# Optimization experiments

Measured on AMD Instinct MI355X. Metric: run time of the kernel, lower is better.

Reference implementation:

```python
import jax, jax.numpy as jnp
import numpy as np

EPS = 1e-6  # torch GaussianNLLLoss default eps


def _linear_params(key, in_size, out_size):
    # torch nn.Linear default init: U(-1/sqrt(in), 1/sqrt(in)) for W and b
    kw, kb = jax.random.split(key)
    bound = 1.0 / np.sqrt(in_size)
    W = jax.random.uniform(kw, (out_size, in_size), minval=-bound, maxval=bound, dtype=jnp.float32)
    b = jax.random.uniform(kb, (out_size,), minval=-bound, maxval=bound, dtype=jnp.float32)
    return W, b


def setup_inputs() -> dict:
    key = jax.random.key(0)
    B, IN, H = 32768, 512, 512
    ks = jax.random.split(key, 6)
    x = jax.random.normal(ks[0], (B, IN), dtype=jnp.float32)
    y = jax.random.normal(ks[1], (B, IN), dtype=jnp.float32)
    W_mu_x, b_mu_x = _linear_params(ks[2], IN, H)
    W_sg_x, b_sg_x = _linear_params(ks[3], IN, H)
    W_mu_y, b_mu_y = _linear_params(ks[4], IN, H)
    W_sg_y, b_sg_y = _linear_params(ks[5], IN, H)
    return {"x": x, "y": y,
            "W_mu_x": W_mu_x, "b_mu_x": b_mu_x,
            "W_sg_x": W_sg_x, "b_sg_x": b_sg_x,
            "W_mu_y": W_mu_y, "b_mu_y": b_mu_y,
            "W_sg_y": W_sg_y, "b_sg_y": b_sg_y}


def _gaussian_nll(xi, mean, var):
    # torch GaussianNLLLoss (full=False, reduction='mean'):
    # mean over features of 0.5*(log(max(var,eps)) + (xi-mean)^2/max(var,eps))
    v = jnp.maximum(var, EPS)
    return 0.5 * jnp.mean(jnp.log(v) + (xi - mean) ** 2 / v)


def _sample_row(key, mx, my, vx, vy):
    # rejection sampling: draw u~U(0,1), xi~U(-1,1); accept when u >= q(xi)
    def cond(c):
        return jnp.logical_not(c[2])

    def body(c):
        k = c[0]
        k, k1, k2 = jax.random.split(k, 3)
        u = jax.random.uniform(k1, dtype=jnp.float32)
        xi = 2.0 * jax.random.uniform(k2, dtype=jnp.float32) - 1.0
        q = _gaussian_nll(xi, mx, vx) * _gaussian_nll(xi, my, vy)
        return (k, xi, u >= q)

    _, xi, _ = jax.lax.while_loop(cond, body, (key, jnp.float32(0.0), jnp.bool_(False)))
    return xi


def reference(x, y, W_mu_x, b_mu_x, W_sg_x, b_sg_x, W_mu_y, b_mu_y, W_sg_y, b_sg_y):
    mean_x = x @ W_mu_x.T + b_mu_x          # [B, H]
    mean_y = y @ W_mu_y.T + b_mu_y          # [B, H]
    std_x = jnp.exp(x @ W_sg_x.T + b_sg_x)  # [B, H] (used as 'var' in GaussianNLLLoss)
    std_y = jnp.exp(y @ W_sg_y.T + b_sg_y)  # [B, H]
    B = x.shape[0]
    keys = jax.random.split(jax.random.key(42), B)
    X = jax.vmap(_sample_row)(keys, mean_x, mean_y, std_x, std_y)  # [B]
    return jnp.clip(X, 1e-5, 10.0)
```

## Files before the change

kernel.cpp:

```cpp
#include <hip/hip_runtime.h>
#include <stdint.h>
#include <math.h>


typedef _Float16 f16;
typedef __attribute__((ext_vector_type(8))) _Float16 f16x8;
typedef __attribute__((ext_vector_type(4))) _Float16 f16x4;
typedef __attribute__((ext_vector_type(4))) float f32x4;

#define SX 16.0f
#define SW 1024.0f
#define INV_S (1.0f / 16384.0f)
#define LOG_EPS (-13.815510557964274f)
#define PLANE 262144
#define WS_NEED (4u * 2u * PLANE * 2u)

struct U2 { uint32_t a, b; };

__device__ __forceinline__ uint32_t rotl(uint32_t v, int d) {
  return (v << d) | (v >> (32 - d));
}

__device__ __forceinline__ U2 tf2x32(uint32_t k0, uint32_t k1, uint32_t x0, uint32_t x1) {
  const uint32_t k2 = k0 ^ k1 ^ 0x1BD11BDAu;
  x0 += k0; x1 += k1;
#define TFR(r) { x0 += x1; x1 = rotl(x1, r); x1 ^= x0; }
  TFR(13) TFR(15) TFR(26) TFR(6)
  x0 += k1; x1 += k2 + 1u;
  TFR(17) TFR(29) TFR(16) TFR(24)
  x0 += k2; x1 += k0 + 2u;
  TFR(13) TFR(15) TFR(26) TFR(6)
  x0 += k0; x1 += k1 + 3u;
  TFR(17) TFR(29) TFR(16) TFR(24)
  x0 += k1; x1 += k2 + 4u;
  TFR(13) TFR(15) TFR(26) TFR(6)
  x0 += k2; x1 += k0 + 5u;
#undef TFR
  U2 r; r.a = x0; r.b = x1; return r;
}

__device__ __forceinline__ float bits_to_u01(uint32_t b) {
  return __uint_as_float((b >> 9) | 0x3f800000u) - 1.0f;
}

__global__ __launch_bounds__(256) void convert_w_kernel(
    const float* __restrict__ w0, const float* __restrict__ w1,
    const float* __restrict__ w2, const float* __restrict__ w3,
    f16* __restrict__ ws)
{
  const int mat = blockIdx.x >> 8;
  const int idx = (((blockIdx.x & 255) << 8) | threadIdx.x) << 2;
  const float* W = (mat == 0) ? w0 : (mat == 1) ? w1 : (mat == 2) ? w2 : w3;
  float4 v = *(const float4*)(W + idx);
  f16* hi = ws + (size_t)mat * (2 * PLANE) + idx;
  f16* lo = hi + PLANE;
  float a0 = v.x * SW, a1 = v.y * SW, a2 = v.z * SW, a3 = v.w * SW;
  f16 h0 = (f16)a0, h1 = (f16)a1, h2 = (f16)a2, h3 = (f16)a3;
  *(f16x4*)hi = (f16x4){h0, h1, h2, h3};
  *(f16x4*)lo = (f16x4){(f16)(a0 - (float)h0), (f16)(a1 - (float)h1),
                        (f16)(a2 - (float)h2), (f16)(a3 - (float)h3)};
}

__device__ __forceinline__ int swz_off(int row, int quad) {
  return row * 32 + ((quad ^ ((row >> 1) & 3)) << 3);
}

__global__ __launch_bounds__(256, 2)
void mfma_proposal_kernel(const float* __restrict__ gx, const float* __restrict__ gy,
                          const float* __restrict__ bmux, const float* __restrict__ bsgx,
                          const float* __restrict__ bmuy, const float* __restrict__ bsgy,
                          const f16* __restrict__ ws, float* __restrict__ out)
{
  __shared__ f16 Xh[64 * 32], Xl[64 * 32];
  __shared__ f16 Wp[4][128 * 32];
  __shared__ double red[4][64][8];

  const int tid = threadIdx.x;
  const int lane = tid & 63;
  const int w = tid >> 6;
  const int ln = lane & 15;
  const int quad = lane >> 4;
  const int r0 = blockIdx.x * 64;

  const int xrow = tid >> 2;
  const int xs4 = tid & 3;
  const int dma_sg = (lane & 3) ^ ((lane >> 3) & 3);
  const int dma_row = lane >> 2;

  for (int i = tid; i < 4 * 64 * 8; i += 256) (&red[0][0][0])[i] = 0.0;

  const float* xbase = gx + (size_t)(r0 + xrow) * 512 + xs4 * 8;
  float4 xr0 = *(const float4*)(xbase);
  float4 xr1 = *(const float4*)(xbase + 4);

  f32x4 accm[4][2], accv[4][2];

  for (int rid = 0; rid < 128; ++rid) {
    const int kc = rid & 15;
    const int cg = (rid >> 4) & 3;
    const int dist = rid >> 6;

    if (kc == 0) {
#pragma unroll
      for (int ri = 0; ri < 4; ++ri)
#pragma unroll
        for (int cj = 0; cj < 2; ++cj) {
          accm[ri][cj] = (f32x4)0.0f;
          accv[ri][cj] = (f32x4)0.0f;
        }
    }

    __syncthreads();

    {
      const f16* plane = ws + (size_t)(dist * 2 + (w >> 1)) * (2 * PLANE)
                            + (size_t)(w & 1) * PLANE;
      const int k0 = kc * 32;
      const int c0 = cg * 128;
      const f16* gp0 = plane + (size_t)(c0 + dma_row) * 512 + k0 + dma_sg * 8;
#pragma unroll
      for (int j = 0; j < 8; ++j) {
        const f16* gp = gp0 + (size_t)(j * 16) * 512;
        f16* lp = &Wp[w][(j * 16) * 32];
        __builtin_amdgcn_global_load_lds(
            (const __attribute__((address_space(1))) void*)gp,
            (__attribute__((address_space(3))) void*)lp, 16, 0, 0);
      }
    }

    {
      const int slot = ((xs4 ^ ((xrow >> 1) & 3)) << 3);
      float a0 = xr0.x * SX, a1 = xr0.y * SX, a2 = xr0.z * SX, a3 = xr0.w * SX;
      float a4 = xr1.x * SX, a5 = xr1.y * SX, a6 = xr1.z * SX, a7 = xr1.w * SX;
      f16 h0 = (f16)a0, h1 = (f16)a1, h2 = (f16)a2, h3 = (f16)a3;
      f16 h4 = (f16)a4, h5 = (f16)a5, h6 = (f16)a6, h7 = (f16)a7;
      *(f16x8*)&Xh[xrow * 32 + slot] = (f16x8){h0, h1, h2, h3, h4, h5, h6, h7};
      *(f16x8*)&Xl[xrow * 32 + slot] =
          (f16x8){(f16)(a0 - (float)h0), (f16)(a1 - (float)h1),
                  (f16)(a2 - (float)h2), (f16)(a3 - (float)h3),
                  (f16)(a4 - (float)h4), (f16)(a5 - (float)h5),
                  (f16)(a6 - (float)h6), (f16)(a7 - (float)h7)};
    }

    __syncthreads();

    if (rid + 1 < 128) {
      const int n = rid + 1;
      const float* Xg = (n >> 6) ? gy : gx;
      const float* xp = Xg + (size_t)(r0 + xrow) * 512 + (n & 15) * 32 + xs4 * 8;
      xr0 = *(const float4*)(xp);
      xr1 = *(const float4*)(xp + 4);
    }

    f16x8 ah[4], al[4];
#pragma unroll
    for (int ri = 0; ri < 4; ++ri) {
      const int off = swz_off(ri * 16 + ln, quad);
      ah[ri] = *(const f16x8*)&Xh[off];
      al[ri] = *(const f16x8*)&Xl[off];
    }
#pragma unroll
    for (int cj = 0; cj < 2; ++cj) {
      const int boff = swz_off(w * 32 + cj * 16 + ln, quad);
      const f16x8 bhm = *(const f16x8*)&Wp[0][boff];
      const f16x8 blm = *(const f16x8*)&Wp[1][boff];
      const f16x8 bhv = *(const f16x8*)&Wp[2][boff];
      const f16x8 blv = *(const f16x8*)&Wp[3][boff];
#pragma unroll
      for (int ri = 0; ri < 4; ++ri) {
        accm[ri][cj] = __builtin_amdgcn_mfma_f32_16x16x32_f16(al[ri], bhm, accm[ri][cj], 0, 0, 0);
        accm[ri][cj] = __builtin_amdgcn_mfma_f32_16x16x32_f16(ah[ri], blm, accm[ri][cj], 0, 0, 0);
        accm[ri][cj] = __builtin_amdgcn_mfma_f32_16x16x32_f16(ah[ri], bhm, accm[ri][cj], 0, 0, 0);
        accv[ri][cj] = __builtin_amdgcn_mfma_f32_16x16x32_f16(al[ri], bhv, accv[ri][cj], 0, 0, 0);
        accv[ri][cj] = __builtin_amdgcn_mfma_f32_16x16x32_f16(ah[ri], blv, accv[ri][cj], 0, 0, 0);
        accv[ri][cj] = __builtin_amdgcn_mfma_f32_16x16x32_f16(ah[ri], bhv, accv[ri][cj], 0, 0, 0);
      }
    }

    if (kc == 15) {
      const float* bmu = dist ? bmuy : bmux;
      const float* bsg = dist ? bsgy : bsgx;
      float bm0 = bmu[cg * 128 + w * 32 + ln];
      float bm1 = bmu[cg * 128 + w * 32 + 16 + ln];
      float bv0 = bsg[cg * 128 + w * 32 + ln];
      float bv1 = bsg[cg * 128 + w * 32 + 16 + ln];
#pragma unroll
      for (int ri = 0; ri < 4; ++ri) {
#pragma unroll
        for (int g = 0; g < 4; ++g) {
          float pA = 0.f, pI = 0.f, pM = 0.f, pQ = 0.f;
#pragma unroll
          for (int cj = 0; cj < 2; ++cj) {
            const float m = accm[ri][cj][g] * INV_S + (cj ? bm1 : bm0);
            const float s = accv[ri][cj][g] * INV_S + (cj ? bv1 : bv0);
            const float vv = fmaxf(expf(s), 1e-6f);
            const float lg = fmaxf(s, LOG_EPS);
            const float iv = __builtin_amdgcn_rcpf(vv);
            pA += lg;
            pI += iv;
            pM += m * iv;
            pQ += m * m * iv;
          }
#pragma unroll
          for (int msk = 1; msk < 16; msk <<= 1) {
            pA += __shfl_xor(pA, msk);
            pI += __shfl_xor(pI, msk);
            pM += __shfl_xor(pM, msk);
            pQ += __shfl_xor(pQ, msk);
          }
          if (ln == 0) {
            double* rr = &red[w][ri * 16 + quad * 4 + g][dist * 4];
            rr[0] += (double)pA; rr[1] += (double)pI;
            rr[2] += (double)pM; rr[3] += (double)pQ;
          }
        }
      }
    }
  }

  __syncthreads();

  if (tid < 64) {
    const int grow = r0 + tid;
    double Ax = 0, Ix = 0, Mx = 0, Qx = 0, Ay = 0, Iy = 0, My = 0, Qy = 0;
#pragma unroll
    for (int s = 0; s < 4; ++s) {
      Ax += red[s][tid][0]; Ix += red[s][tid][1];
      Mx += red[s][tid][2]; Qx += red[s][tid][3];
      Ay += red[s][tid][4]; Iy += red[s][tid][5];
      My += red[s][tid][6]; Qy += red[s][tid][7];
    }

    U2 key = tf2x32(0u, 42u, 0u, (uint32_t)grow);

    float xi = 0.0f;
    bool done = false;
    for (int it = 0; it < 100000 && !done; ++it) {
      const U2 kn = tf2x32(key.a, key.b, 0u, 0u);
      const U2 k1 = tf2x32(key.a, key.b, 0u, 1u);
      const U2 k2 = tf2x32(key.a, key.b, 0u, 2u);
      const U2 ru = tf2x32(k1.a, k1.b, 0u, 0u);
      const U2 rx = tf2x32(k2.a, k2.b, 0u, 0u);
      const float u  = bits_to_u01(ru.a ^ ru.b);
      const float u2 = bits_to_u01(rx.a ^ rx.b);
      xi = 2.0f * u2 - 1.0f;
      const double dxi = (double)xi;
      const double nx = (0.5 / 512.0) * (Ax + Qx + dxi * (dxi * Ix - 2.0 * Mx));
      const double ny = (0.5 / 512.0) * (Ay + Qy + dxi * (dxi * Iy - 2.0 * My));
      done = ((double)u >= nx * ny);
      key = kn;
    }
    out[grow] = fminf(fmaxf(xi, 1e-5f), 10.0f);
  }
}

__global__ __launch_bounds__(256, 1)
void fused_proposal_vec(const float* __restrict__ gx, const float* __restrict__ gy,
                        const float* __restrict__ Wmux, const float* __restrict__ bmux,
                        const float* __restrict__ Wsgx, const float* __restrict__ bsgx,
                        const float* __restrict__ Wmuy, const float* __restrict__ bmuy,
                        const float* __restrict__ Wsgy, const float* __restrict__ bsgy,
                        float* __restrict__ out)
{
  __shared__ float Xs[16][68];
  __shared__ float Wms[16][132];
  __shared__ float Wss[16][132];
  __shared__ double red[64][8];

  const int tid = threadIdx.x;
  const int tx = tid & 15;
  const int ty = tid >> 4;
  const int r0 = blockIdx.x * 64;
  const int lr = tid >> 2;
  const int q4 = (tid & 3) << 2;

  for (int i = tid; i < 64 * 8; i += 256) ((double*)red)[i] = 0.0;

  for (int ph = 0; ph < 8; ++ph) {
    const int dist = ph >> 2;
    const int c0 = (ph & 3) * 128;
    const float* __restrict__ Xg = dist ? gy : gx;
    const float* __restrict__ Wm = dist ? Wmuy : Wmux;
    const float* __restrict__ Wv = dist ? Wsgy : Wsgx;
    const float* __restrict__ bm = dist ? bmuy : bmux;
    const float* __restrict__ bv = dist ? bsgy : bsgx;

    float am[4][8], av[4][8];
#pragma unroll
    for (int r = 0; r < 4; ++r)
#pragma unroll
      for (int c = 0; c < 8; ++c) { am[r][c] = 0.0f; av[r][c] = 0.0f; }

    const float* xp  = Xg + (size_t)(r0 + lr) * 512 + q4;
    const float* mp0 = Wm + (size_t)(c0 + lr) * 512 + q4;
    const float* mp1 = Wm + (size_t)(c0 + lr + 64) * 512 + q4;
    const float* vp0 = Wv + (size_t)(c0 + lr) * 512 + q4;
    const float* vp1 = Wv + (size_t)(c0 + lr + 64) * 512 + q4;

    float4 xa = *(const float4*)(xp);
    float4 ma = *(const float4*)(mp0);
    float4 mb = *(const float4*)(mp1);
    float4 va = *(const float4*)(vp0);
    float4 vb = *(const float4*)(vp1);

    for (int t = 0; t < 32; ++t) {
      __syncthreads();
#define ST4(arr, col, v) { arr[q4+0][col]=v.x; arr[q4+1][col]=v.y; arr[q4+2][col]=v.z; arr[q4+3][col]=v.w; }
      ST4(Xs,  lr, xa)
      ST4(Wms, lr, ma)  ST4(Wms, lr + 64, mb)
      ST4(Wss, lr, va)  ST4(Wss, lr + 64, vb)
#undef ST4
      __syncthreads();
      if (t + 1 < 32) {
        const int ko = (t + 1) * 16;
        xa = *(const float4*)(xp + ko);
        ma = *(const float4*)(mp0 + ko);
        mb = *(const float4*)(mp1 + ko);
        va = *(const float4*)(vp0 + ko);
        vb = *(const float4*)(vp1 + ko);
      }
#pragma unroll
      for (int kk = 0; kk < 16; ++kk) {
        const float4 x0 = *(const float4*)&Xs[kk][ty * 4];
        const float4 m0 = *(const float4*)&Wms[kk][tx * 4];
        const float4 m1 = *(const float4*)&Wms[kk][tx * 4 + 64];
        const float4 v0 = *(const float4*)&Wss[kk][tx * 4];
        const float4 v1 = *(const float4*)&Wss[kk][tx * 4 + 64];
        const float xr[4] = {x0.x, x0.y, x0.z, x0.w};
        const float wm[8] = {m0.x, m0.y, m0.z, m0.w, m1.x, m1.y, m1.z, m1.w};
        const float wv[8] = {v0.x, v0.y, v0.z, v0.w, v1.x, v1.y, v1.z, v1.w};
#pragma unroll
        for (int r = 0; r < 4; ++r)
#pragma unroll
          for (int c = 0; c < 8; ++c) {
            am[r][c] = fmaf(xr[r], wm[c], am[r][c]);
            av[r][c] = fmaf(xr[r], wv[c], av[r][c]);
          }
      }
    }

    float bmr[8], bvr[8];
#pragma unroll
    for (int c = 0; c < 4; ++c) {
      bmr[c]     = bm[c0 + tx * 4 + c];
      bmr[4 + c] = bm[c0 + 64 + tx * 4 + c];
      bvr[c]     = bv[c0 + tx * 4 + c];
      bvr[4 + c] = bv[c0 + 64 + tx * 4 + c];
    }
#pragma unroll
    for (int r = 0; r < 4; ++r) {
      float pA = 0.f, pI = 0.f, pM = 0.f, pQ = 0.f;
#pragma unroll
      for (int c = 0; c < 8; ++c) {
        const float m = am[r][c] + bmr[c];
        const float s = av[r][c] + bvr[c];
        const float v = fmaxf(expf(s), 1e-6f);
        const float lg = fmaxf(s, LOG_EPS);
        const float inv = __builtin_amdgcn_rcpf(v);
        pA += lg; pI += inv; pM += m * inv; pQ += m * m * inv;
      }
#pragma unroll
      for (int msk = 1; msk < 16; msk <<= 1) {
        pA += __shfl_xor(pA, msk);
        pI += __shfl_xor(pI, msk);
        pM += __shfl_xor(pM, msk);
        pQ += __shfl_xor(pQ, msk);
      }
      if (tx == 0) {
        double* rr = &red[ty * 4 + r][dist * 4];
        rr[0] += (double)pA; rr[1] += (double)pI;
        rr[2] += (double)pM; rr[3] += (double)pQ;
      }
    }
  }

  __syncthreads();

  if (tid < 64) {
    const int grow = r0 + tid;
    const double Ax = red[tid][0], Ix = red[tid][1], Mx = red[tid][2], Qx = red[tid][3];
    const double Ay = red[tid][4], Iy = red[tid][5], My = red[tid][6], Qy = red[tid][7];
    U2 key = tf2x32(0u, 42u, 0u, (uint32_t)grow);
    float xi = 0.0f;
    bool done = false;
    for (int it = 0; it < 100000 && !done; ++it) {
      const U2 kn = tf2x32(key.a, key.b, 0u, 0u);
      const U2 k1 = tf2x32(key.a, key.b, 0u, 1u);
      const U2 k2 = tf2x32(key.a, key.b, 0u, 2u);
      const U2 ru = tf2x32(k1.a, k1.b, 0u, 0u);
      const U2 rx = tf2x32(k2.a, k2.b, 0u, 0u);
      const float u  = bits_to_u01(ru.a ^ ru.b);
      const float u2 = bits_to_u01(rx.a ^ rx.b);
      xi = 2.0f * u2 - 1.0f;
      const double dxi = (double)xi;
      const double nx = (0.5 / 512.0) * (Ax + Qx + dxi * (dxi * Ix - 2.0 * Mx));
      const double ny = (0.5 / 512.0) * (Ay + Qy + dxi * (dxi * Iy - 2.0 * My));
      done = ((double)u >= nx * ny);
      key = kn;
    }
    out[grow] = fminf(fmaxf(xi, 1e-5f), 10.0f);
  }
}

extern "C" void kernel_launch(void* const* d_in, const int* in_sizes, int n_in,
                              void* d_out, int out_size, void* d_ws, size_t ws_size,
                              hipStream_t stream) {
  const float* x    = (const float*)d_in[0];
  const float* y    = (const float*)d_in[1];
  const float* Wmux = (const float*)d_in[2];
  const float* bmux = (const float*)d_in[3];
  const float* Wsgx = (const float*)d_in[4];
  const float* bsgx = (const float*)d_in[5];
  const float* Wmuy = (const float*)d_in[6];
  const float* bmuy = (const float*)d_in[7];
  const float* Wsgy = (const float*)d_in[8];
  const float* bsgy = (const float*)d_in[9];
  (void)in_sizes; (void)n_in; (void)out_size;

  if (ws_size >= (size_t)WS_NEED) {
    convert_w_kernel<<<1024, 256, 0, stream>>>(Wmux, Wsgx, Wmuy, Wsgy, (f16*)d_ws);
    mfma_proposal_kernel<<<512, 256, 0, stream>>>(
        x, y, bmux, bsgx, bmuy, bsgy, (const f16*)d_ws, (float*)d_out);
  } else {
    fused_proposal_vec<<<512, 256, 0, stream>>>(
        x, y, Wmux, bmux, Wsgx, bsgx, Wmuy, bmuy, Wsgy, bsgy, (float*)d_out);
  }
}
```

Measured before the change: 394.4 us.

## Double-buffer weight and input tiles in LDS, keep row reductions in registers

Adds ping-pong LDS buffers for the weight and split-f16 input tiles, so the next k-chunk is staged while the current one is consumed by MFMA. This replaces the two barriers per iteration with a single wait plus barrier. The per-row statistics are now kept in double registers on a designated lane instead of being added into a shared reduction array, and that array is aliased onto the weight buffer at the end. LDS use per block roughly doubles, which may limit the two-blocks-per-CU occupancy target, and the explicit vmcnt(0) wait still serialises on the prefetch.

```diff
diff --git a/kernel.cpp b/kernel.cpp
--- a/kernel.cpp
+++ b/kernel.cpp
@@ -71,9 +71,9 @@
                           const float* __restrict__ bmuy, const float* __restrict__ bsgy,
                           const f16* __restrict__ ws, float* __restrict__ out)
 {
-  __shared__ f16 Xh[64 * 32], Xl[64 * 32];
-  __shared__ f16 Wp[4][128 * 32];
-  __shared__ double red[4][64][8];
+  __shared__ __align__(16) f16 Wp[2][4][128 * 32];
+  __shared__ __align__(16) f16 Xh[2][64 * 32];
+  __shared__ __align__(16) f16 Xl[2][64 * 32];
 
   const int tid = threadIdx.x;
   const int lane = tid & 63;
@@ -86,16 +86,57 @@
   const int xs4 = tid & 3;
   const int dma_sg = (lane & 3) ^ ((lane >> 3) & 3);
   const int dma_row = lane >> 2;
-
-  for (int i = tid; i < 4 * 64 * 8; i += 256) (&red[0][0][0])[i] = 0.0;
-
-  const float* xbase = gx + (size_t)(r0 + xrow) * 512 + xs4 * 8;
-  float4 xr0 = *(const float4*)(xbase);
-  float4 xr1 = *(const float4*)(xbase + 4);
+  const int xslot = (xs4 ^ ((xrow >> 1) & 3)) << 3;
+
+  double dAx = 0, dIx = 0, dMx = 0, dQx = 0;
+  double dAy = 0, dIy = 0, dMy = 0, dQy = 0;
+
+  float4 xr0, xr1;
+
+  auto load_xr = [&](int n) {
+    const float* Xg = (n >> 6) ? gy : gx;
+    const float* xp = Xg + (size_t)(r0 + xrow) * 512 + (n & 15) * 32 + xs4 * 8;
+    xr0 = *(const float4*)(xp);
+    xr1 = *(const float4*)(xp + 4);
+  };
+
+  auto stage_w = [&](int n, int buf) {
+    const int nkc = n & 15, ncg = (n >> 4) & 3, nd = n >> 6;
+    const f16* plane = ws + (size_t)(nd * 2 + (w >> 1)) * (2 * PLANE)
+                          + (size_t)(w & 1) * PLANE;
+    const f16* gp0 = plane + (size_t)(ncg * 128 + dma_row) * 512 + nkc * 32 + dma_sg * 8;
+#pragma unroll
+    for (int j = 0; j < 8; ++j) {
+      __builtin_amdgcn_global_load_lds(
+          (const __attribute__((address_space(1))) void*)(gp0 + (size_t)(j * 16) * 512),
+          (__attribute__((address_space(3))) void*)&Wp[buf][w][(j * 16) * 32], 16, 0, 0);
+    }
+  };
+
+  auto write_x = [&](int buf) {
+    float a0 = xr0.x * SX, a1 = xr0.y * SX, a2 = xr0.z * SX, a3 = xr0.w * SX;
+    float a4 = xr1.x * SX, a5 = xr1.y * SX, a6 = xr1.z * SX, a7 = xr1.w * SX;
+    f16 h0 = (f16)a0, h1 = (f16)a1, h2 = (f16)a2, h3 = (f16)a3;
+    f16 h4 = (f16)a4, h5 = (f16)a5, h6 = (f16)a6, h7 = (f16)a7;
+    *(f16x8*)&Xh[buf][xrow * 32 + xslot] = (f16x8){h0, h1, h2, h3, h4, h5, h6, h7};
+    *(f16x8*)&Xl[buf][xrow * 32 + xslot] =
+        (f16x8){(f16)(a0 - (float)h0), (f16)(a1 - (float)h1),
+                (f16)(a2 - (float)h2), (f16)(a3 - (float)h3),
+                (f16)(a4 - (float)h4), (f16)(a5 - (float)h5),
+                (f16)(a6 - (float)h6), (f16)(a7 - (float)h7)};
+  };
+
+  load_xr(0);
+  stage_w(0, 0);
+  write_x(0);
+  load_xr(1);
+  __syncthreads();
 
   f32x4 accm[4][2], accv[4][2];
 
   for (int rid = 0; rid < 128; ++rid) {
+    const int cb = rid & 1;
+    const int nb = cb ^ 1;
     const int kc = rid & 15;
     const int cg = (rid >> 4) & 3;
     const int dist = rid >> 6;
@@ -110,62 +151,26 @@
         }
     }
 
-    __syncthreads();
-
-    {
-      const f16* plane = ws + (size_t)(dist * 2 + (w >> 1)) * (2 * PLANE)
-                            + (size_t)(w & 1) * PLANE;
-      const int k0 = kc * 32;
-      const int c0 = cg * 128;
-      const f16* gp0 = plane + (size_t)(c0 + dma_row) * 512 + k0 + dma_sg * 8;
-#pragma unroll
-      for (int j = 0; j < 8; ++j) {
-        const f16* gp = gp0 + (size_t)(j * 16) * 512;
-        f16* lp = &Wp[w][(j * 16) * 32];
-        __builtin_amdgcn_global_load_lds(
-            (const __attribute__((address_space(1))) void*)gp,
-            (__attribute__((address_space(3))) void*)lp, 16, 0, 0);
-      }
-    }
-
-    {
-      const int slot = ((xs4 ^ ((xrow >> 1) & 3)) << 3);
-      float a0 = xr0.x * SX, a1 = xr0.y * SX, a2 = xr0.z * SX, a3 = xr0.w * SX;
-      float a4 = xr1.x * SX, a5 = xr1.y * SX, a6 = xr1.z * SX, a7 = xr1.w * SX;
-      f16 h0 = (f16)a0, h1 = (f16)a1, h2 = (f16)a2, h3 = (f16)a3;
-      f16 h4 = (f16)a4, h5 = (f16)a5, h6 = (f16)a6, h7 = (f16)a7;
-      *(f16x8*)&Xh[xrow * 32 + slot] = (f16x8){h0, h1, h2, h3, h4, h5, h6, h7};
-      *(f16x8*)&Xl[xrow * 32 + slot] =
-          (f16x8){(f16)(a0 - (float)h0), (f16)(a1 - (float)h1),
-                  (f16)(a2 - (float)h2), (f16)(a3 - (float)h3),
-                  (f16)(a4 - (float)h4), (f16)(a5 - (float)h5),
-                  (f16)(a6 - (float)h6), (f16)(a7 - (float)h7)};
-    }
-
-    __syncthreads();
-
     if (rid + 1 < 128) {
-      const int n = rid + 1;
-      const float* Xg = (n >> 6) ? gy : gx;
-      const float* xp = Xg + (size_t)(r0 + xrow) * 512 + (n & 15) * 32 + xs4 * 8;
-      xr0 = *(const float4*)(xp);
-      xr1 = *(const float4*)(xp + 4);
-    }
+      stage_w(rid + 1, nb);
+      write_x(nb);
+    }
+    if (rid + 2 < 128) load_xr(rid + 2);
 
     f16x8 ah[4], al[4];
 #pragma unroll
     for (int ri = 0; ri < 4; ++ri) {
       const int off = swz_off(ri * 16 + ln, quad);
-      ah[ri] = *(const f16x8*)&Xh[off];
-      al[ri] = *(const f16x8*)&Xl[off];
+      ah[ri] = *(const f16x8*)&Xh[cb][off];
+      al[ri] = *(const f16x8*)&Xl[cb][off];
     }
 #pragma unroll
     for (int cj = 0; cj < 2; ++cj) {
       const int boff = swz_off(w * 32 + cj * 16 + ln, quad);
-      const f16x8 bhm = *(const f16x8*)&Wp[0][boff];
-      const f16x8 blm = *(const f16x8*)&Wp[1][boff];
-      const f16x8 bhv = *(const f16x8*)&Wp[2][boff];
-      const f16x8 blv = *(const f16x8*)&Wp[3][boff];
+      const f16x8 bhm = *(const f16x8*)&Wp[cb][0][boff];
+      const f16x8 blm = *(const f16x8*)&Wp[cb][1][boff];
+      const f16x8 bhv = *(const f16x8*)&Wp[cb][2][boff];
+      const f16x8 blv = *(const f16x8*)&Wp[cb][3][boff];
 #pragma unroll
       for (int ri = 0; ri < 4; ++ri) {
         accm[ri][cj] = __builtin_amdgcn_mfma_f32_16x16x32_f16(al[ri], bhm, accm[ri][cj], 0, 0, 0);
@@ -180,10 +185,10 @@
     if (kc == 15) {
       const float* bmu = dist ? bmuy : bmux;
       const float* bsg = dist ? bsgy : bsgx;
-      float bm0 = bmu[cg * 128 + w * 32 + ln];
-      float bm1 = bmu[cg * 128 + w * 32 + 16 + ln];
-      float bv0 = bsg[cg * 128 + w * 32 + ln];
-      float bv1 = bsg[cg * 128 + w * 32 + 16 + ln];
+      const float bm0 = bmu[cg * 128 + w * 32 + ln];
+      const float bm1 = bmu[cg * 128 + w * 32 + 16 + ln];
+      const float bv0 = bsg[cg * 128 + w * 32 + ln];
+      const float bv1 = bsg[cg * 128 + w * 32 + 16 + ln];
 #pragma unroll
       for (int ri = 0; ri < 4; ++ri) {
 #pragma unroll
@@ -208,16 +213,27 @@
             pM += __shfl_xor(pM, msk);
             pQ += __shfl_xor(pQ, msk);
           }
-          if (ln == 0) {
-            double* rr = &red[w][ri * 16 + quad * 4 + g][dist * 4];
-            rr[0] += (double)pA; rr[1] += (double)pI;
-            rr[2] += (double)pM; rr[3] += (double)pQ;
+          if (ln == ri * 4 + g) {
+            if (dist == 0) { dAx += pA; dIx += pI; dMx += pM; dQx += pQ; }
+            else           { dAy += pA; dIy += pI; dMy += pM; dQy += pQ; }
           }
         }
       }
     }
-  }
-
+
+    asm volatile("s_waitcnt vmcnt(0)" ::: "memory");
+    asm volatile("s_waitcnt lgkmcnt(0)" ::: "memory");
+    __builtin_amdgcn_s_barrier();
+  }
+
+  __syncthreads();
+  double* red = (double*)&Wp[0][0][0];
+  {
+    const int myrow = (ln >> 2) * 16 + quad * 4 + (ln & 3);
+    double* rr = red + (size_t)(w * 64 + myrow) * 8;
+    rr[0] = dAx; rr[1] = dIx; rr[2] = dMx; rr[3] = dQx;
+    rr[4] = dAy; rr[5] = dIy; rr[6] = dMy; rr[7] = dQy;
+  }
   __syncthreads();
 
   if (tid < 64) {
@@ -225,10 +241,9 @@
     double Ax = 0, Ix = 0, Mx = 0, Qx = 0, Ay = 0, Iy = 0, My = 0, Qy = 0;
 #pragma unroll
     for (int s = 0; s < 4; ++s) {
-      Ax += red[s][tid][0]; Ix += red[s][tid][1];
-      Mx += red[s][tid][2]; Qx += red[s][tid][3];
-      Ay += red[s][tid][4]; Iy += red[s][tid][5];
-      My += red[s][tid][6]; Qy += red[s][tid][7];
+      const double* rr = red + (size_t)(s * 64 + tid) * 8;
+      Ax += rr[0]; Ix += rr[1]; Mx += rr[2]; Qx += rr[3];
+      Ay += rr[4]; Iy += rr[5]; My += rr[6]; Qy += rr[7];
     }
 
     U2 key = tf2x32(0u, 42u, 0u, (uint32_t)grow);
```

New measurement: 430.3 us. +9.1%, slower.

## Pre-swizzle weights into MFMA fragment layout and load B operands directly to registers

Applied to the files above, without the earlier changes.

The weight conversion kernel now writes the f16 hi/lo split in the exact per-lane MFMA B-fragment order. The main kernel therefore drops the LDS weight staging buffer and the global_load_lds DMA, loading B fragments straight into registers. These loads are double-buffered, so the next round's fragments are fetched while the current round's MFMAs run. This removes LDS traffic and shared memory for weights, which may raise occupancy. The cost is more VGPRs for the two fragment buffers and every wave reading its fragments from global/L2 memory.

```diff
diff --git a/kernel.cpp b/kernel.cpp
--- a/kernel.cpp
+++ b/kernel.cpp
@@ -5,7 +5,6 @@
 
 typedef _Float16 f16;
 typedef __attribute__((ext_vector_type(8))) _Float16 f16x8;
-typedef __attribute__((ext_vector_type(4))) _Float16 f16x4;
 typedef __attribute__((ext_vector_type(4))) float f32x4;
 
 #define SX 16.0f
@@ -14,6 +13,13 @@
 #define LOG_EPS (-13.815510557964274f)
 #define PLANE 262144
 #define WS_NEED (4u * 2u * PLANE * 2u)
+
+#define KC_S   512
+#define CJ_S   8192
+#define WV_S   16384
+#define CG_S   65536
+#define HILO_S 262144
+#define MAT_S  524288
 
 struct U2 { uint32_t a, b; };
 
@@ -48,17 +54,34 @@
     const float* __restrict__ w2, const float* __restrict__ w3,
     f16* __restrict__ ws)
 {
-  const int mat = blockIdx.x >> 8;
-  const int idx = (((blockIdx.x & 255) << 8) | threadIdx.x) << 2;
+  const int t = blockIdx.x * 256 + threadIdx.x;
+  const int mat = t >> 15;
+  const int r = t & 32767;
+  const int lane = r & 63;
+  const int kc = (r >> 6) & 15;
+  const int cj = (r >> 10) & 1;
+  const int wv = (r >> 11) & 3;
+  const int cg = (r >> 13) & 3;
+  const int ln = lane & 15, quad = lane >> 4;
+  const int row = cg * 128 + wv * 32 + cj * 16 + ln;
+  const int k0 = kc * 32 + quad * 8;
   const float* W = (mat == 0) ? w0 : (mat == 1) ? w1 : (mat == 2) ? w2 : w3;
-  float4 v = *(const float4*)(W + idx);
-  f16* hi = ws + (size_t)mat * (2 * PLANE) + idx;
-  f16* lo = hi + PLANE;
-  float a0 = v.x * SW, a1 = v.y * SW, a2 = v.z * SW, a3 = v.w * SW;
-  f16 h0 = (f16)a0, h1 = (f16)a1, h2 = (f16)a2, h3 = (f16)a3;
-  *(f16x4*)hi = (f16x4){h0, h1, h2, h3};
-  *(f16x4*)lo = (f16x4){(f16)(a0 - (float)h0), (f16)(a1 - (float)h1),
-                        (f16)(a2 - (float)h2), (f16)(a3 - (float)h3)};
+  const float* p = W + (size_t)row * 512 + k0;
+  const float4 va = *(const float4*)p;
+  const float4 vb = *(const float4*)(p + 4);
+  const float a[8] = {va.x, va.y, va.z, va.w, vb.x, vb.y, vb.z, vb.w};
+  f16x8 h, l;
+#pragma unroll
+  for (int i = 0; i < 8; ++i) {
+    const float ai = a[i] * SW;
+    const f16 hi = (f16)ai;
+    h[i] = hi;
+    l[i] = (f16)(ai - (float)hi);
+  }
+  f16* dst = ws + (size_t)mat * MAT_S + (size_t)cg * CG_S + (size_t)wv * WV_S
+                + (size_t)cj * CJ_S + (size_t)kc * KC_S + (size_t)lane * 8;
+  *(f16x8*)dst = h;
+  *(f16x8*)(dst + HILO_S) = l;
 }
 
 __device__ __forceinline__ int swz_off(int row, int quad) {
@@ -72,7 +95,6 @@
                           const f16* __restrict__ ws, float* __restrict__ out)
 {
   __shared__ f16 Xh[64 * 32], Xl[64 * 32];
-  __shared__ f16 Wp[4][128 * 32];
   __shared__ double red[4][64][8];
 
   const int tid = threadIdx.x;
@@ -84,18 +106,53 @@
 
   const int xrow = tid >> 2;
   const int xs4 = tid & 3;
-  const int dma_sg = (lane & 3) ^ ((lane >> 3) & 3);
-  const int dma_row = lane >> 2;
+  const int xslot = (xs4 ^ ((xrow >> 1) & 3)) << 3;
 
   for (int i = tid; i < 4 * 64 * 8; i += 256) (&red[0][0][0])[i] = 0.0;
 
-  const float* xbase = gx + (size_t)(r0 + xrow) * 512 + xs4 * 8;
-  float4 xr0 = *(const float4*)(xbase);
-  float4 xr1 = *(const float4*)(xbase + 4);
-
+  const f16* wbase = ws + (size_t)w * WV_S + (size_t)lane * 8;
+
+  float4 xr0, xr1;
+  auto load_xr = [&](int n) {
+    const float* Xg = (n >> 6) ? gy : gx;
+    const float* xp = Xg + (size_t)(r0 + xrow) * 512 + (n & 15) * 32 + xs4 * 8;
+    xr0 = *(const float4*)(xp);
+    xr1 = *(const float4*)(xp + 4);
+  };
+
+  auto write_x = [&]() {
+    float a0 = xr0.x * SX, a1 = xr0.y * SX, a2 = xr0.z * SX, a3 = xr0.w * SX;
+    float a4 = xr1.x * SX, a5 = xr1.y * SX, a6 = xr1.z * SX, a7 = xr1.w * SX;
+    f16 h0 = (f16)a0, h1 = (f16)a1, h2 = (f16)a2, h3 = (f16)a3;
+    f16 h4 = (f16)a4, h5 = (f16)a5, h6 = (f16)a6, h7 = (f16)a7;
+    *(f16x8*)&Xh[xrow * 32 + xslot] = (f16x8){h0, h1, h2, h3, h4, h5, h6, h7};
+    *(f16x8*)&Xl[xrow * 32 + xslot] =
+        (f16x8){(f16)(a0 - (float)h0), (f16)(a1 - (float)h1),
+                (f16)(a2 - (float)h2), (f16)(a3 - (float)h3),
+                (f16)(a4 - (float)h4), (f16)(a5 - (float)h5),
+                (f16)(a6 - (float)h6), (f16)(a7 - (float)h7)};
+  };
+
+  auto load_W = [&](int n, f16x8 (&B)[4][2]) {
+    const int kc = n & 15, cg = (n >> 4) & 3, d = n >> 6;
+    const f16* base = wbase + (size_t)(d * 2) * MAT_S + (size_t)cg * CG_S
+                            + (size_t)kc * KC_S;
+#pragma unroll
+    for (int p = 0; p < 4; ++p)
+#pragma unroll
+      for (int cj = 0; cj < 2; ++cj)
+        B[p][cj] = *(const f16x8*)(base + (size_t)(p >> 1) * MAT_S
+                                        + (size_t)(p & 1) * HILO_S
+                                        + (size_t)cj * CJ_S);
+  };
+
+  f16x8 Ba[4][2], Bb[4][2];
   f32x4 accm[4][2], accv[4][2];
 
-  for (int rid = 0; rid < 128; ++rid) {
+  load_xr(0);
+  load_W(0, Ba);
+
+  auto round_fn = [&](int rid, f16x8 (&Bc)[4][2], f16x8 (&Bn)[4][2]) {
     const int kc = rid & 15;
     const int cg = (rid >> 4) & 3;
     const int dist = rid >> 6;
@@ -111,45 +168,12 @@
     }
 
     __syncthreads();
-
-    {
-      const f16* plane = ws + (size_t)(dist * 2 + (w >> 1)) * (2 * PLANE)
-                            + (size_t)(w & 1) * PLANE;
-      const int k0 = kc * 32;
-      const int c0 = cg * 128;
-      const f16* gp0 = plane + (size_t)(c0 + dma_row) * 512 + k0 + dma_sg * 8;
-#pragma unroll
-      for (int j = 0; j < 8; ++j) {
-        const f16* gp = gp0 + (size_t)(j * 16) * 512;
-        f16* lp = &Wp[w][(j * 16) * 32];
-        __builtin_amdgcn_global_load_lds(
-            (const __attribute__((address_space(1))) void*)gp,
-            (__attribute__((address_space(3))) void*)lp, 16, 0, 0);
-      }
-    }
-
-    {
-      const int slot = ((xs4 ^ ((xrow >> 1) & 3)) << 3);
-      float a0 = xr0.x * SX, a1 = xr0.y * SX, a2 = xr0.z * SX, a3 = xr0.w * SX;
-      float a4 = xr1.x * SX, a5 = xr1.y * SX, a6 = xr1.z * SX, a7 = xr1.w * SX;
-      f16 h0 = (f16)a0, h1 = (f16)a1, h2 = (f16)a2, h3 = (f16)a3;
-      f16 h4 = (f16)a4, h5 = (f16)a5, h6 = (f16)a6, h7 = (f16)a7;
-      *(f16x8*)&Xh[xrow * 32 + slot] = (f16x8){h0, h1, h2, h3, h4, h5, h6, h7};
-      *(f16x8*)&Xl[xrow * 32 + slot] =
-          (f16x8){(f16)(a0 - (float)h0), (f16)(a1 - (float)h1),
-                  (f16)(a2 - (float)h2), (f16)(a3 - (float)h3),
-                  (f16)(a4 - (float)h4), (f16)(a5 - (float)h5),
-                  (f16)(a6 - (float)h6), (f16)(a7 - (float)h7)};
-    }
-
+    write_x();
     __syncthreads();
 
     if (rid + 1 < 128) {
-      const int n = rid + 1;
-      const float* Xg = (n >> 6) ? gy : gx;
-      const float* xp = Xg + (size_t)(r0 + xrow) * 512 + (n & 15) * 32 + xs4 * 8;
-      xr0 = *(const float4*)(xp);
-      xr1 = *(const float4*)(xp + 4);
+      load_xr(rid + 1);
+      load_W(rid + 1, Bn);
     }
 
     f16x8 ah[4], al[4];
@@ -161,11 +185,10 @@
     }
 #pragma unroll
     for (int cj = 0; cj < 2; ++cj) {
-      const int boff = swz_off(w * 32 + cj * 16 + ln, quad);
-      const f16x8 bhm = *(const f16x8*)&Wp[0][boff];
-      const f16x8 blm = *(const f16x8*)&Wp[1][boff];
-      const f16x8 bhv = *(const f16x8*)&Wp[2][boff];
-      const f16x8 blv = *(const f16x8*)&Wp[3][boff];
+      const f16x8 bhm = Bc[0][cj];
+      const f16x8 blm = Bc[1][cj];
+      const f16x8 bhv = Bc[2][cj];
+      const f16x8 blv = Bc[3][cj];
 #pragma unroll
       for (int ri = 0; ri < 4; ++ri) {
         accm[ri][cj] = __builtin_amdgcn_mfma_f32_16x16x32_f16(al[ri], bhm, accm[ri][cj], 0, 0, 0);
@@ -216,6 +239,11 @@
         }
       }
     }
+  };
+
+  for (int rr = 0; rr < 64; ++rr) {
+    round_fn(rr * 2,     Ba, Bb);
+    round_fn(rr * 2 + 1, Bb, Ba);
   }
 
   __syncthreads();
@@ -418,7 +446,7 @@
   (void)in_sizes; (void)n_in; (void)out_size;
 
   if (ws_size >= (size_t)WS_NEED) {
-    convert_w_kernel<<<1024, 256, 0, stream>>>(Wmux, Wsgx, Wmuy, Wsgy, (f16*)d_ws);
+    convert_w_kernel<<<512, 256, 0, stream>>>(Wmux, Wsgx, Wmuy, Wsgy, (f16*)d_ws);
     mfma_proposal_kernel<<<512, 256, 0, stream>>>(
         x, y, bmux, bsgx, bmuy, bsgy, (const f16*)d_ws, (float*)d_out);
   } else {
```

Result: faster. 367.8 us (-6.8%).
